# Kernel optimization log

Measured on AMD Instinct MI355X. Metric: run time of the kernel, lower is better.

## Reference

```python
import jax, jax.numpy as jnp
import numpy as np

EPS = 1e-6  # flax nnx LayerNorm default

def _ln(x):
    # LayerNorm without scale/bias
    m = jnp.mean(x, axis=-1, keepdims=True)
    v = jnp.mean(jnp.square(x - m), axis=-1, keepdims=True)
    return (x - m) * jax.lax.rsqrt(v + EPS)

def _modulate(x, shift, scale):
    return x * (1.0 + scale[:, None]) + shift[:, None]

def setup_inputs() -> dict:
    key = jax.random.key(0)
    B, S, H, NH = 8, 1024, 1024, 16
    ks = jax.random.split(key, 12)
    s = lambda k, sh: jax.random.normal(k, sh, dtype=jnp.float32) * 0.02
    return {
        "x": jax.random.normal(ks[0], (B, S, H), dtype=jnp.float32),
        "c": jax.random.normal(ks[1], (B, H), dtype=jnp.float32),
        "w_ada": s(ks[2], (H, 6 * H)),
        "b_ada": jnp.zeros((6 * H,), dtype=jnp.float32),
        "w_qkv": s(ks[3], (H, 3 * H)),
        "w_proj": s(ks[4], (H, H)),
        "b_proj": jnp.zeros((H,), dtype=jnp.float32),
        "w_mlp1": s(ks[5], (H, 4 * H)),
        "b_mlp1": jnp.zeros((4 * H,), dtype=jnp.float32),
        "w_mlp2": s(ks[6], (4 * H, H)),
        "b_mlp2": jnp.zeros((H,), dtype=jnp.float32),
    }

def reference(x, c, w_ada, b_ada, w_qkv, w_proj, b_proj, w_mlp1, b_mlp1, w_mlp2, b_mlp2):
    B, S, H = x.shape
    NH = 16
    CH = H // NH
    # adaLN modulation: silu -> Linear
    cmod = jax.nn.silu(c) @ w_ada + b_ada  # [B, 6H]
    shift_msa, scale_msa, gate_msa, shift_mlp, scale_mlp, gate_mlp = jnp.split(cmod, 6, axis=-1)
    # attention branch
    x_mod = _modulate(_ln(x), shift_msa, scale_msa)
    qkv = x_mod @ w_qkv  # [B, S, 3H]
    k, q, v = jnp.split(qkv, 3, axis=-1)  # note source order: k, q, v
    k = k.reshape(B, S, NH, CH)
    q = q.reshape(B, S, NH, CH)
    v = v.reshape(B, S, NH, CH)
    q = q / CH  # faithful: divide by head_dim (not sqrt)
    w = jnp.einsum('bqhc,bkhc->bhqk', q, k).astype(jnp.float32)
    w = jax.nn.softmax(w, axis=-1)
    y = jnp.einsum('bhqk,bkhc->bqhc', w, v).reshape(B, S, H)
    attn_x = y @ w_proj + b_proj
    x = x + gate_msa[:, None] * attn_x
    # MLP branch
    x_mod2 = _modulate(_ln(x), shift_mlp, scale_mlp)
    h = jax.nn.gelu(x_mod2 @ w_mlp1 + b_mlp1)
    mlp_x = h @ w_mlp2 + b_mlp2
    x = x + gate_mlp[:, None] * mlp_x
    return x
```

## Files before the change

kernel.cpp:

```cpp
#include <hip/hip_runtime.h>
#include <stdint.h>

typedef unsigned short u16;
using bf16x8 = __attribute__((ext_vector_type(8))) __bf16;
using f32x4  = __attribute__((ext_vector_type(4))) float;

#define MFMA16(a,b,c) __builtin_amdgcn_mfma_f32_16x16x32_bf16((a),(b),(c),0,0,0)

__device__ __forceinline__ u16 f2bf(float f) {
  union { float f; uint32_t u; } v; v.f = f;
  uint32_t r = v.u + 0x7FFFu + ((v.u >> 16) & 1u);
  return (u16)(r >> 16);
}
__device__ __forceinline__ float bf2f(u16 u) {
  union { uint32_t u; float f; } v; v.u = ((uint32_t)u) << 16;
  return v.f;
}

__device__ __forceinline__ void gload_lds16(const void* g, void* l) {
  typedef const __attribute__((address_space(1))) void* gp_t;
  typedef __attribute__((address_space(3))) void* lp_t;
  __builtin_amdgcn_global_load_lds((gp_t)(uintptr_t)g,
                                   (lp_t)(uint32_t)(uintptr_t)l, 16, 0, 0);
}

__global__ __launch_bounds__(256)
void prep_k(const float* __restrict__ w_qkv, const float* __restrict__ w_proj,
            const float* __restrict__ w_mlp1, const float* __restrict__ w_mlp2,
            u16* __restrict__ oq, u16* __restrict__ op,
            u16* __restrict__ o1, u16* __restrict__ o2,
            const float* __restrict__ c, const float* __restrict__ w_ada,
            float* __restrict__ partial) {
  int bid = blockIdx.x;
  if (bid >= 3072) {
    bid -= 3072;
    const int jb = bid % 24, ks = bid / 24;
    const int j = jb * 256 + threadIdx.x;
    __shared__ float sil[8][32];
    {
      int b = threadIdx.x >> 5, kk = threadIdx.x & 31;
      float v = c[b * 1024 + ks * 32 + kk];
      sil[b][kk] = v / (1.f + __expf(-v));
    }
    __syncthreads();
    float acc[8] = {0,0,0,0,0,0,0,0};
#pragma unroll 8
    for (int kk = 0; kk < 32; ++kk) {
      float wv = w_ada[(size_t)(ks * 32 + kk) * 6144 + j];
#pragma unroll
      for (int b = 0; b < 8; ++b) acc[b] += sil[b][kk] * wv;
    }
#pragma unroll
    for (int b = 0; b < 8; ++b)
      partial[((size_t)ks * 8 + b) * 6144 + j] = acc[b];
    return;
  }
  const float* in; u16* out; int K, N, lo = 0, hi = 0;
  float scale = 1.0f;
  if (bid < 768)       { in = w_qkv;  out = oq; K = 1024; N = 3072;
                         lo = 1024; hi = 2048; scale = 1.0f / 64.0f; }
  else if (bid < 1024) { in = w_proj; out = op; K = 1024; N = 1024; bid -= 768; }
  else if (bid < 2048) { in = w_mlp1; out = o1; K = 1024; N = 4096; bid -= 1024; }
  else                 { in = w_mlp2; out = o2; K = 4096; N = 1024; bid -= 2048; }
  const int nbx = N >> 6;
  const int n0 = (bid % nbx) * 64, k0 = (bid / nbx) * 64;
  __shared__ u16 t[64][65];
#pragma unroll
  for (int i = 0; i < 16; ++i) {
    int idx = i * 256 + threadIdx.x;
    int r = idx >> 6, cc = idx & 63;
    float v = in[(size_t)(k0 + r) * N + n0 + cc];
    int n = n0 + cc;
    if (n >= lo && n < hi) v *= scale;
    t[r][cc] = f2bf(v);
  }
  __syncthreads();
#pragma unroll
  for (int i = 0; i < 16; ++i) {
    int idx = i * 256 + threadIdx.x;
    int r = idx >> 6, cc = idx & 63;
    out[(size_t)(n0 + r) * K + k0 + cc] = t[cc][r];
  }
}

__global__ __launch_bounds__(256)
void adaln_red_k(const float* __restrict__ partial, const float* __restrict__ bias,
                 float* __restrict__ cmod) {
  int g = blockIdx.x * 256 + threadIdx.x;
  int j = g % 6144;
  float s = bias[j];
#pragma unroll 8
  for (int ks = 0; ks < 32; ++ks)
    s += partial[(size_t)ks * 8 * 6144 + g];
  cmod[g] = s;
}

__global__ __launch_bounds__(256)
void lnmod_k(const float* __restrict__ x, const float* __restrict__ cmod,
             int shift_off, int scale_off, u16* __restrict__ out) {
  int row = blockIdx.x;
  int b = row >> 10;
  const float4* xr = (const float4*)(x + (size_t)row * 1024);
  float4 v = xr[threadIdx.x];
  float s = v.x + v.y + v.z + v.w;
  float sq = v.x * v.x + v.y * v.y + v.z * v.z + v.w * v.w;
#pragma unroll
  for (int m = 32; m >= 1; m >>= 1) {
    s  += __shfl_xor(s, m);
    sq += __shfl_xor(sq, m);
  }
  __shared__ float ss[4], ssq[4];
  int wave = threadIdx.x >> 6, lane = threadIdx.x & 63;
  if (lane == 0) { ss[wave] = s; ssq[wave] = sq; }
  __syncthreads();
  s  = ss[0] + ss[1] + ss[2] + ss[3];
  sq = ssq[0] + ssq[1] + ssq[2] + ssq[3];
  float mean = s * (1.f / 1024.f);
  float var  = sq * (1.f / 1024.f) - mean * mean;
  float rstd = rsqrtf(var + 1e-6f);
  int col = threadIdx.x * 4;
  const float* sh = cmod + (size_t)b * 6144 + shift_off + col;
  const float* sc = cmod + (size_t)b * 6144 + scale_off + col;
  float xv[4] = {v.x, v.y, v.z, v.w};
  union { u16 o[4]; uint64_t u; } pk;
#pragma unroll
  for (int j = 0; j < 4; ++j)
    pk.o[j] = f2bf((xv[j] - mean) * rstd * (1.f + sc[j]) + sh[j]);
  *(uint64_t*)(out + (size_t)row * 1024 + col) = pk.u;
}

__global__ __launch_bounds__(256)
void lnmodb_k(const u16* __restrict__ x, const float* __restrict__ cmod,
              int shift_off, int scale_off, u16* __restrict__ out) {
  int row = blockIdx.x;
  int b = row >> 10;
  ushort4 v4 = *(const ushort4*)(x + (size_t)row * 1024 + threadIdx.x * 4);
  float xv[4] = {bf2f(v4.x), bf2f(v4.y), bf2f(v4.z), bf2f(v4.w)};
  float s = xv[0] + xv[1] + xv[2] + xv[3];
  float sq = xv[0]*xv[0] + xv[1]*xv[1] + xv[2]*xv[2] + xv[3]*xv[3];
#pragma unroll
  for (int m = 32; m >= 1; m >>= 1) {
    s  += __shfl_xor(s, m);
    sq += __shfl_xor(sq, m);
  }
  __shared__ float ss[4], ssq[4];
  int wave = threadIdx.x >> 6, lane = threadIdx.x & 63;
  if (lane == 0) { ss[wave] = s; ssq[wave] = sq; }
  __syncthreads();
  s  = ss[0] + ss[1] + ss[2] + ss[3];
  sq = ssq[0] + ssq[1] + ssq[2] + ssq[3];
  float mean = s * (1.f / 1024.f);
  float var  = sq * (1.f / 1024.f) - mean * mean;
  float rstd = rsqrtf(var + 1e-6f);
  int col = threadIdx.x * 4;
  const float* sh = cmod + (size_t)b * 6144 + shift_off + col;
  const float* sc = cmod + (size_t)b * 6144 + scale_off + col;
  union { u16 o[4]; uint64_t u; } pk;
#pragma unroll
  for (int j = 0; j < 4; ++j)
    pk.o[j] = f2bf((xv[j] - mean) * rstd * (1.f + sc[j]) + sh[j]);
  *(uint64_t*)(out + (size_t)row * 1024 + col) = pk.u;
}

__device__ __forceinline__ float gelu_f(float x) {
  float z = 1.5957691216057308f * (x + 0.044715f * x * x * x);
  return x / (1.f + __expf(-z));
}

template <int EP>
__global__ __launch_bounds__(256)
void gemm_k(const u16* __restrict__ A, const u16* __restrict__ Bt,
            int N, int K,
            const float* __restrict__ bias, const void* __restrict__ residp,
            const float* __restrict__ gate, void* __restrict__ outp) {
  __shared__ __align__(16) u16 lds[3][2][128 * 32];
  const int bn = blockIdx.x, bm = blockIdx.y;
  const int tid = threadIdx.x;
  const int wave = tid >> 6, lane = tid & 63;
  const int l15 = lane & 15, lhi = lane >> 4;
  const int wr = wave >> 1, wc = wave & 1;
  f32x4 acc[4][4] = {};
  const int nkt = K >> 5;
  const size_t arow0 = (size_t)bm * 128;
  const size_t brow0 = (size_t)bn * 128;

  auto stage = [&](int buf, int kt) {
#pragma unroll
    for (int i = 0; i < 2; ++i) {
      int c = (i * 4 + wave) * 64 + lane;
      int row = c >> 2;
      int kc = (c & 3) ^ ((row >> 1) & 3);
      gload_lds16(A  + (arow0 + row) * K + (size_t)kt * 32 + kc * 8,
                  &lds[buf][0][(i * 4 + wave) * 512]);
      gload_lds16(Bt + (brow0 + row) * K + (size_t)kt * 32 + kc * 8,
                  &lds[buf][1][(i * 4 + wave) * 512]);
    }
  };
  auto compute = [&](int buf) {
    bf16x8 af[4], bfr[4];
#pragma unroll
    for (int m = 0; m < 4; ++m) {
      int r = wr * 64 + m * 16 + l15;
      af[m] = *(const bf16x8*)&lds[buf][0][r * 32 + (lhi ^ ((r >> 1) & 3)) * 8];
    }
#pragma unroll
    for (int n = 0; n < 4; ++n) {
      int r = wc * 64 + n * 16 + l15;
      bfr[n] = *(const bf16x8*)&lds[buf][1][r * 32 + (lhi ^ ((r >> 1) & 3)) * 8];
    }
#pragma unroll
    for (int m = 0; m < 4; ++m)
#pragma unroll
      for (int n = 0; n < 4; ++n)
        acc[m][n] = MFMA16(af[m], bfr[n], acc[m][n]);
  };

  stage(0, 0);
  stage(1, 1);
  asm volatile("s_waitcnt vmcnt(4)" ::: "memory");
  __builtin_amdgcn_s_barrier();
  asm volatile("" ::: "memory");

  for (int t = 0; t < nkt; ++t) {
    const int cur = t % 3;
    const bool pf2 = (t + 2 < nkt);
    if (pf2) stage((t + 2) % 3, t + 2);
    compute(cur);
    if (t + 1 < nkt) {
      if (pf2) asm volatile("s_waitcnt vmcnt(4)" ::: "memory");
      else     asm volatile("s_waitcnt vmcnt(0)" ::: "memory");
      __builtin_amdgcn_s_barrier();
      asm volatile("" ::: "memory");
    }
  }

#pragma unroll
  for (int m = 0; m < 4; ++m) {
    int row = bm * 128 + wr * 64 + m * 16 + lhi * 4;
#pragma unroll
    for (int n = 0; n < 4; ++n) {
      int col = bn * 128 + wc * 64 + n * 16 + l15;
      if (EP == 0 && col >= 2048) {
        int h = (col - 2048) >> 6, ch = (col - 2048) & 63;
        int b = row >> 10, s0 = row & 1023;
        u16* vt = (u16*)residp;
        union { u16 o[4]; uint64_t u; } pk;
#pragma unroll
        for (int r = 0; r < 4; ++r) pk.o[r] = f2bf(acc[m][n][r]);
        *(uint64_t*)&vt[((size_t)(b * 16 + h) * 64 + ch) * 1024 + s0] = pk.u;
        continue;
      }
#pragma unroll
      for (int r = 0; r < 4; ++r) {
        int rr = row + r;
        float v = acc[m][n][r];
        if (EP == 0) {
          ((u16*)outp)[(size_t)rr * N + col] = f2bf(v);
        } else if (EP == 1) {
          ((u16*)outp)[(size_t)rr * N + col] = f2bf(gelu_f(v + bias[col]));
        } else if (EP == 2) {
          float t2 = v + bias[col];
          int b = rr >> 10;
          float res = ((const float*)residp)[(size_t)rr * N + col];
          ((u16*)outp)[(size_t)rr * N + col] =
              f2bf(res + gate[(size_t)b * 6144 + col] * t2);
        } else {
          float t2 = v + bias[col];
          int b = rr >> 10;
          float res = bf2f(((const u16*)residp)[(size_t)rr * N + col]);
          ((float*)outp)[(size_t)rr * N + col] = res + gate[(size_t)b * 6144 + col] * t2;
        }
      }
    }
  }
}

__global__ __launch_bounds__(256)
void attn_k(const u16* __restrict__ qkv, const u16* __restrict__ vt,
            u16* __restrict__ y) {
  int bid0 = blockIdx.x + 16 * (blockIdx.y + 16 * blockIdx.z);
  int swz = (bid0 & 7) * 256 + (bid0 >> 3);
  const int qt = swz & 15, h = (swz >> 4) & 15, b = swz >> 8;
  const int tid = threadIdx.x, wave = tid >> 6, lane = tid & 63;
  const int l15 = lane & 15, lhi = lane >> 4;
  __shared__ __align__(16) u16 Qs[64 * 64];
  __shared__ __align__(16) u16 Ks[2][64 * 64];
  __shared__ __align__(16) u16 Vs[2][64 * 64];
  __shared__ __align__(16) u16 Ps[64 * 64];
  const size_t qrow0 = (size_t)b * 1024 + qt * 64;
  const size_t krow0 = (size_t)b * 1024;
  const size_t vrow0 = (size_t)(b * 16 + h) * 64;

  auto stageQ = [&]() {
#pragma unroll
    for (int i = 0; i < 2; ++i) {
      int c = (i * 4 + wave) * 64 + lane;
      int r = c >> 3, j = (c & 7) ^ (r & 7);
      gload_lds16(qkv + (qrow0 + r) * 3072 + 1024 + h * 64 + j * 8,
                  &Qs[(i * 4 + wave) * 512]);
    }
  };
  auto stageKV = [&](int buf, int kt) {
#pragma unroll
    for (int i = 0; i < 2; ++i) {
      int c = (i * 4 + wave) * 64 + lane;
      int r = c >> 3, j = (c & 7) ^ (r & 7);
      gload_lds16(qkv + (krow0 + kt * 64 + r) * 3072 + h * 64 + j * 8,
                  &Ks[buf][(i * 4 + wave) * 512]);
      gload_lds16(vt + (vrow0 + r) * 1024 + kt * 64 + j * 8,
                  &Vs[buf][(i * 4 + wave) * 512]);
    }
  };
  auto ldb = [](const u16* base, int row, int cc) -> bf16x8 {
    return *(const bf16x8*)&base[row * 64 + ((cc ^ (row & 7)) << 3)];
  };

  stageQ();
  stageKV(0, 0);
  __syncthreads();
  bf16x8 qf[2];
  qf[0] = ldb(Qs, wave * 16 + l15, lhi);
  qf[1] = ldb(Qs, wave * 16 + l15, 4 + lhi);

  bf16x8 ones;
#pragma unroll
  for (int j = 0; j < 8; ++j) ones[j] = (__bf16)1.0f;

  f32x4 o[5] = {};

  for (int kt = 0; kt < 16; ++kt) {
    int cur = kt & 1;
    if (kt < 15) stageKV(cur ^ 1, kt + 1);
    f32x4 sf[4] = {};
    __builtin_amdgcn_s_setprio(1);
#pragma unroll
    for (int n = 0; n < 4; ++n) {
      bf16x8 k0 = ldb(Ks[cur], n * 16 + l15, lhi);
      bf16x8 k1 = ldb(Ks[cur], n * 16 + l15, 4 + lhi);
      sf[n] = MFMA16(qf[0], k0, sf[n]);
      sf[n] = MFMA16(qf[1], k1, sf[n]);
    }
    __builtin_amdgcn_s_setprio(0);
#pragma unroll
    for (int r = 0; r < 4; ++r) {
      int row = wave * 16 + lhi * 4 + r;
      int rb = row * 64, sw = (row & 7) << 3;
      Ps[rb + (l15 ^ sw)]        = f2bf(__expf(sf[0][r]));
      Ps[rb + ((l15 + 16) ^ sw)] = f2bf(__expf(sf[1][r]));
      Ps[rb + ((l15 + 32) ^ sw)] = f2bf(__expf(sf[2][r]));
      Ps[rb + ((l15 + 48) ^ sw)] = f2bf(__expf(sf[3][r]));
    }
    bf16x8 pf0 = ldb(Ps, wave * 16 + l15, lhi);
    bf16x8 pf1 = ldb(Ps, wave * 16 + l15, 4 + lhi);
    __builtin_amdgcn_s_setprio(1);
#pragma unroll
    for (int n = 0; n < 4; ++n) {
      bf16x8 v0 = ldb(Vs[cur], n * 16 + l15, lhi);
      bf16x8 v1 = ldb(Vs[cur], n * 16 + l15, 4 + lhi);
      o[n] = MFMA16(pf0, v0, o[n]);
      o[n] = MFMA16(pf1, v1, o[n]);
    }
    o[4] = MFMA16(pf0, ones, o[4]);
    o[4] = MFMA16(pf1, ones, o[4]);
    __builtin_amdgcn_s_setprio(0);
    __syncthreads();
  }
#pragma unroll
  for (int r = 0; r < 4; ++r) {
    float inv = 1.0f / o[4][r];
    size_t yrow = (qrow0 + wave * 16 + lhi * 4 + r) * 1024 + h * 64 + l15;
    y[yrow]      = f2bf(o[0][r] * inv);
    y[yrow + 16] = f2bf(o[1][r] * inv);
    y[yrow + 32] = f2bf(o[2][r] * inv);
    y[yrow + 48] = f2bf(o[3][r] * inv);
  }
}

extern "C" void kernel_launch(void* const* d_in, const int* in_sizes, int n_in,
                              void* d_out, int out_size, void* d_ws, size_t ws_size,
                              hipStream_t stream) {
  const float* x      = (const float*)d_in[0];
  const float* c      = (const float*)d_in[1];
  const float* w_ada  = (const float*)d_in[2];
  const float* b_ada  = (const float*)d_in[3];
  const float* w_qkv  = (const float*)d_in[4];
  const float* w_proj = (const float*)d_in[5];
  const float* b_proj = (const float*)d_in[6];
  const float* w_mlp1 = (const float*)d_in[7];
  const float* b_mlp1 = (const float*)d_in[8];
  const float* w_mlp2 = (const float*)d_in[9];
  const float* b_mlp2 = (const float*)d_in[10];
  float* out = (float*)d_out;

  char* ws = (char*)d_ws;
  size_t off = 0;
  auto alloc = [&](size_t bytes) {
    void* p = ws + off;
    off += (bytes + 255) & ~(size_t)255;
    return p;
  };
  float* cmod  = (float*)alloc((size_t)8 * 6144 * 4);
  float* apart = (float*)alloc((size_t)32 * 8 * 6144 * 4);
  u16* wqkvT   = (u16*)alloc((size_t)3072 * 1024 * 2);
  u16* wprojT  = (u16*)alloc((size_t)1024 * 1024 * 2);
  u16* wmlp1T  = (u16*)alloc((size_t)4096 * 1024 * 2);
  u16* wmlp2T  = (u16*)alloc((size_t)1024 * 4096 * 2);
  u16* xmod    = (u16*)alloc((size_t)8192 * 1024 * 2);
  u16* qkv     = (u16*)alloc((size_t)8192 * 3072 * 2);
  u16* vt      = (u16*)alloc((size_t)8 * 16 * 64 * 1024 * 2);
  u16* x1      = (u16*)alloc((size_t)8192 * 1024 * 2);
  u16* hbuf    = (u16*)alloc((size_t)8192 * 4096 * 2);
  u16* ybuf  = xmod;
  u16* xmod2 = qkv;

  prep_k<<<3840, 256, 0, stream>>>(w_qkv, w_proj, w_mlp1, w_mlp2,
                                   wqkvT, wprojT, wmlp1T, wmlp2T,
                                   c, w_ada, apart);
  adaln_red_k<<<192, 256, 0, stream>>>(apart, b_ada, cmod);
  lnmod_k<<<8192, 256, 0, stream>>>(x, cmod, 0, 1024, xmod);
  gemm_k<0><<<dim3(3072 / 128, 8192 / 128), 256, 0, stream>>>(
      xmod, wqkvT, 3072, 1024, nullptr, vt, nullptr, qkv);
  attn_k<<<dim3(16, 16, 8), 256, 0, stream>>>(qkv, vt, ybuf);
  gemm_k<2><<<dim3(1024 / 128, 8192 / 128), 256, 0, stream>>>(
      ybuf, wprojT, 1024, 1024, b_proj, x, cmod + 2048, x1);
  lnmodb_k<<<8192, 256, 0, stream>>>(x1, cmod, 3072, 4096, xmod2);
  gemm_k<1><<<dim3(4096 / 128, 8192 / 128), 256, 0, stream>>>(
      xmod2, wmlp1T, 4096, 1024, b_mlp1, nullptr, nullptr, hbuf);
  gemm_k<3><<<dim3(1024 / 128, 8192 / 128), 256, 0, stream>>>(
      hbuf, wmlp2T, 1024, 4096, b_mlp2, x1, cmod + 5120, out);
}
```

Measured before the change: 388.4 us.

## Load GEMM A fragments directly from global into registers, keep only B in LDS

The GEMM kernel stops staging the A tile in shared memory. Each wave now loads its A fragments straight from global memory into registers, while B is still staged through LDS. The three-buffer pipeline with explicit vmcnt waits becomes a double buffer using __syncthreads, unrolled by two. This cuts LDS footprint and LDS read traffic, but A is re-read from global or L2 by both column waves, the global loads are less coalesced, and latency hiding is shallower.

```diff
diff --git a/kernel.cpp b/kernel.cpp
--- a/kernel.cpp
+++ b/kernel.cpp
@@ -173,7 +173,7 @@
             int N, int K,
             const float* __restrict__ bias, const void* __restrict__ residp,
             const float* __restrict__ gate, void* __restrict__ outp) {
-  __shared__ __align__(16) u16 lds[3][2][128 * 32];
+  __shared__ __align__(16) u16 Bs[2][128 * 32];
   const int bn = blockIdx.x, bm = blockIdx.y;
   const int tid = threadIdx.x;
   const int wave = tid >> 6, lane = tid & 63;
@@ -184,30 +184,31 @@
   const size_t arow0 = (size_t)bm * 128;
   const size_t brow0 = (size_t)bn * 128;
 
-  auto stage = [&](int buf, int kt) {
+  const u16* abase[4];
+#pragma unroll
+  for (int m = 0; m < 4; ++m)
+    abase[m] = A + (arow0 + wr * 64 + m * 16 + l15) * (size_t)K + lhi * 8;
+
+  auto stageB = [&](int buf, int kt) {
 #pragma unroll
     for (int i = 0; i < 2; ++i) {
-      int c = (i * 4 + wave) * 64 + lane;
-      int row = c >> 2;
-      int kc = (c & 3) ^ ((row >> 1) & 3);
-      gload_lds16(A  + (arow0 + row) * K + (size_t)kt * 32 + kc * 8,
-                  &lds[buf][0][(i * 4 + wave) * 512]);
+      int cch = (i * 4 + wave) * 64 + lane;
+      int row = cch >> 2;
+      int kc = (cch & 3) ^ ((row >> 1) & 3);
       gload_lds16(Bt + (brow0 + row) * K + (size_t)kt * 32 + kc * 8,
-                  &lds[buf][1][(i * 4 + wave) * 512]);
-    }
-  };
-  auto compute = [&](int buf) {
-    bf16x8 af[4], bfr[4];
-#pragma unroll
-    for (int m = 0; m < 4; ++m) {
-      int r = wr * 64 + m * 16 + l15;
-      af[m] = *(const bf16x8*)&lds[buf][0][r * 32 + (lhi ^ ((r >> 1) & 3)) * 8];
-    }
-#pragma unroll
-    for (int n = 0; n < 4; ++n) {
-      int r = wc * 64 + n * 16 + l15;
-      bfr[n] = *(const bf16x8*)&lds[buf][1][r * 32 + (lhi ^ ((r >> 1) & 3)) * 8];
-    }
+                  &Bs[buf][(i * 4 + wave) * 512]);
+    }
+  };
+  int offB[4];
+#pragma unroll
+  for (int n = 0; n < 4; ++n) {
+    int r = wc * 64 + n * 16 + l15;
+    offB[n] = r * 32 + (lhi ^ ((r >> 1) & 3)) * 8;
+  }
+  auto computeB = [&](int buf, const bf16x8* af) {
+    bf16x8 bfr[4];
+#pragma unroll
+    for (int n = 0; n < 4; ++n) bfr[n] = *(const bf16x8*)&Bs[buf][offB[n]];
 #pragma unroll
     for (int m = 0; m < 4; ++m)
 #pragma unroll
@@ -215,23 +216,27 @@
         acc[m][n] = MFMA16(af[m], bfr[n], acc[m][n]);
   };
 
-  stage(0, 0);
-  stage(1, 1);
-  asm volatile("s_waitcnt vmcnt(4)" ::: "memory");
-  __builtin_amdgcn_s_barrier();
-  asm volatile("" ::: "memory");
-
-  for (int t = 0; t < nkt; ++t) {
-    const int cur = t % 3;
-    const bool pf2 = (t + 2 < nkt);
-    if (pf2) stage((t + 2) % 3, t + 2);
-    compute(cur);
-    if (t + 1 < nkt) {
-      if (pf2) asm volatile("s_waitcnt vmcnt(4)" ::: "memory");
-      else     asm volatile("s_waitcnt vmcnt(0)" ::: "memory");
-      __builtin_amdgcn_s_barrier();
-      asm volatile("" ::: "memory");
-    }
+  bf16x8 afA[4], afB[4];
+#pragma unroll
+  for (int m = 0; m < 4; ++m) afA[m] = *(const bf16x8*)(abase[m]);
+  stageB(0, 0);
+  __syncthreads();
+
+  for (int t = 0; t < nkt; t += 2) {
+    stageB(1, t + 1);
+#pragma unroll
+    for (int m = 0; m < 4; ++m)
+      afB[m] = *(const bf16x8*)(abase[m] + (t + 1) * 32);
+    computeB(0, afA);
+    __syncthreads();
+    if (t + 2 < nkt) {
+      stageB(0, t + 2);
+#pragma unroll
+      for (int m = 0; m < 4; ++m)
+        afA[m] = *(const bf16x8*)(abase[m] + (t + 2) * 32);
+    }
+    computeB(1, afB);
+    __syncthreads();
   }
 
 #pragma unroll
```

Result: slower. 619.3 us (+59.4%).

## Add 256x256-tile 8-wave ping-pong GEMM for MLP1 with GELU epilogue

Applied to the files above, without the earlier changes.

Adds a new GEMM kernel with 256x256 output tiles, 512 threads (8 waves), and a double-buffered global-to-LDS pipeline that interleaves LDS fragment loads, prefetch of k+2 tiles, and MFMA phases under barriers and s_setprio. It replaces the 128x128 gemm_k<1> for the MLP1 projection (8192x4096x1024), which is the largest GEMM. The larger tile is meant to raise arithmetic intensity and cut global and LDS traffic per FLOP. In exchange it runs one workgroup per CU with 512 blocks total, and the epilogue writes scalar bf16 stores.

```diff
diff --git a/kernel.cpp b/kernel.cpp
--- a/kernel.cpp
+++ b/kernel.cpp
@@ -275,6 +275,165 @@
   }
 }
 
+__global__ __launch_bounds__(512, 1)
+void gemm8_k(const u16* __restrict__ A, const u16* __restrict__ Bt,
+             int N, int K,
+             const float* __restrict__ bias, u16* __restrict__ outp) {
+  __shared__ __align__(16) u16 As[2][256 * 64];
+  __shared__ __align__(16) u16 Bs[2][256 * 64];
+  const int nwg = gridDim.x * gridDim.y;
+  int bid = blockIdx.y * gridDim.x + blockIdx.x;
+  int swz = (bid & 7) * (nwg >> 3) + (bid >> 3);
+  const int bn = swz % gridDim.x, bm = swz / gridDim.x;
+  const int tid = threadIdx.x;
+  const int wave = tid >> 6, lane = tid & 63;
+  const int l15 = lane & 15, lhi = lane >> 4;
+  const int wm = wave >> 2, wn = wave & 3;
+  const int nkt = K >> 6;
+  const size_t arow0 = (size_t)bm * 256;
+  const size_t brow0 = (size_t)bn * 256;
+
+  f32x4 acc[2][4][4] = {};
+
+  auto stage_half = [&](const u16* mat, size_t row0, u16* dst, int kt) {
+    const u16* src = mat + row0 * K + (size_t)kt * 64;
+#pragma unroll
+    for (int i = 0; i < 2; ++i) {
+      int q = i * 512 + tid;
+      int r = q >> 3, cc = (q & 7) ^ (r & 7);
+      gload_lds16(src + (size_t)r * K + cc * 8, dst + (i * 8 + wave) * 512);
+    }
+  };
+  auto lda = [&](int cur, int row, int kh) -> bf16x8 {
+    int cc = (kh * 4 + lhi) ^ (row & 7);
+    return *(const bf16x8*)&As[cur][row * 64 + cc * 8];
+  };
+  auto ldbf = [&](int cur, int row, int kh) -> bf16x8 {
+    int cc = (kh * 4 + lhi) ^ (row & 7);
+    return *(const bf16x8*)&Bs[cur][row * 64 + cc * 8];
+  };
+
+#define PH_BAR()  do { asm volatile("" ::: "memory"); __builtin_amdgcn_s_barrier(); \
+                       asm volatile("" ::: "memory"); } while (0)
+#define PH_LGKM() do { asm volatile("s_waitcnt lgkmcnt(0)" ::: "memory"); \
+                       __builtin_amdgcn_sched_barrier(0); } while (0)
+
+  stage_half(A,  arow0,       &As[0][0],        0);
+  stage_half(A,  arow0 + 128, &As[0][128 * 64], 0);
+  stage_half(Bt, brow0,       &Bs[0][0],        0);
+  stage_half(Bt, brow0 + 128, &Bs[0][128 * 64], 0);
+  stage_half(A,  arow0,       &As[1][0],        1);
+  stage_half(A,  arow0 + 128, &As[1][128 * 64], 1);
+  stage_half(Bt, brow0,       &Bs[1][0],        1);
+  stage_half(Bt, brow0 + 128, &Bs[1][128 * 64], 1);
+  asm volatile("s_waitcnt vmcnt(8)" ::: "memory");
+  PH_BAR();
+
+  bf16x8 afr[4][2], bfr01[2][2], bfr23[2][2];
+  for (int kt = 0; kt < nkt; ++kt) {
+    const int cur = kt & 1;
+    const bool pf2 = (kt + 2 < nkt);
+
+#pragma unroll
+    for (int m = 0; m < 4; ++m) {
+      int r = wm * 128 + m * 16 + l15;
+      afr[m][0] = lda(cur, r, 0); afr[m][1] = lda(cur, r, 1);
+    }
+#pragma unroll
+    for (int n = 0; n < 2; ++n) {
+      int r = wn * 64 + n * 16 + l15;
+      bfr01[n][0] = ldbf(cur, r, 0); bfr01[n][1] = ldbf(cur, r, 1);
+    }
+    PH_BAR(); PH_LGKM();
+    __builtin_amdgcn_s_setprio(1);
+#pragma unroll
+    for (int m = 0; m < 4; ++m)
+#pragma unroll
+      for (int n = 0; n < 2; ++n) {
+        acc[0][m][n] = MFMA16(afr[m][0], bfr01[n][0], acc[0][m][n]);
+        acc[0][m][n] = MFMA16(afr[m][1], bfr01[n][1], acc[0][m][n]);
+      }
+    __builtin_amdgcn_s_setprio(0);
+    PH_BAR();
+
+#pragma unroll
+    for (int n = 0; n < 2; ++n) {
+      int r = wn * 64 + (n + 2) * 16 + l15;
+      bfr23[n][0] = ldbf(cur, r, 0); bfr23[n][1] = ldbf(cur, r, 1);
+    }
+    PH_BAR(); PH_LGKM();
+    __builtin_amdgcn_s_setprio(1);
+#pragma unroll
+    for (int m = 0; m < 4; ++m)
+#pragma unroll
+      for (int n = 0; n < 2; ++n) {
+        acc[0][m][n + 2] = MFMA16(afr[m][0], bfr23[n][0], acc[0][m][n + 2]);
+        acc[0][m][n + 2] = MFMA16(afr[m][1], bfr23[n][1], acc[0][m][n + 2]);
+      }
+    __builtin_amdgcn_s_setprio(0);
+    PH_BAR();
+
+#pragma unroll
+    for (int m = 0; m < 4; ++m) {
+      int r = wm * 128 + 64 + m * 16 + l15;
+      afr[m][0] = lda(cur, r, 0); afr[m][1] = lda(cur, r, 1);
+    }
+    if (pf2) {
+      stage_half(Bt, brow0,       &Bs[cur][0],        kt + 2);
+      stage_half(Bt, brow0 + 128, &Bs[cur][128 * 64], kt + 2);
+    }
+    PH_BAR(); PH_LGKM();
+    __builtin_amdgcn_s_setprio(1);
+#pragma unroll
+    for (int m = 0; m < 4; ++m)
+#pragma unroll
+      for (int n = 0; n < 2; ++n) {
+        acc[1][m][n] = MFMA16(afr[m][0], bfr01[n][0], acc[1][m][n]);
+        acc[1][m][n] = MFMA16(afr[m][1], bfr01[n][1], acc[1][m][n]);
+      }
+    __builtin_amdgcn_s_setprio(0);
+    PH_BAR();
+
+    if (pf2) {
+      stage_half(A, arow0,       &As[cur][0],        kt + 2);
+      stage_half(A, arow0 + 128, &As[cur][128 * 64], kt + 2);
+    }
+    PH_BAR();
+    __builtin_amdgcn_s_setprio(1);
+#pragma unroll
+    for (int m = 0; m < 4; ++m)
+#pragma unroll
+      for (int n = 0; n < 2; ++n) {
+        acc[1][m][n + 2] = MFMA16(afr[m][0], bfr23[n][0], acc[1][m][n + 2]);
+        acc[1][m][n + 2] = MFMA16(afr[m][1], bfr23[n][1], acc[1][m][n + 2]);
+      }
+    __builtin_amdgcn_s_setprio(0);
+    if (kt + 1 < nkt) {
+      if (pf2) asm volatile("s_waitcnt vmcnt(8)" ::: "memory");
+      else     asm volatile("s_waitcnt vmcnt(0)" ::: "memory");
+      PH_BAR();
+    }
+  }
+#undef PH_BAR
+#undef PH_LGKM
+
+#pragma unroll
+  for (int mh = 0; mh < 2; ++mh)
+#pragma unroll
+    for (int m = 0; m < 4; ++m) {
+      int row = bm * 256 + wm * 128 + mh * 64 + m * 16 + lhi * 4;
+#pragma unroll
+      for (int n = 0; n < 4; ++n) {
+        int col = bn * 256 + wn * 64 + n * 16 + l15;
+#pragma unroll
+        for (int r = 0; r < 4; ++r) {
+          int rr = row + r;
+          outp[(size_t)rr * N + col] = f2bf(gelu_f(acc[mh][m][n][r] + bias[col]));
+        }
+      }
+    }
+}
+
 __global__ __launch_bounds__(256)
 void attn_k(const u16* __restrict__ qkv, const u16* __restrict__ vt,
             u16* __restrict__ y) {
@@ -424,8 +583,8 @@
   gemm_k<2><<<dim3(1024 / 128, 8192 / 128), 256, 0, stream>>>(
       ybuf, wprojT, 1024, 1024, b_proj, x, cmod + 2048, x1);
   lnmodb_k<<<8192, 256, 0, stream>>>(x1, cmod, 3072, 4096, xmod2);
-  gemm_k<1><<<dim3(4096 / 128, 8192 / 128), 256, 0, stream>>>(
-      xmod2, wmlp1T, 4096, 1024, b_mlp1, nullptr, nullptr, hbuf);
+  gemm8_k<<<dim3(4096 / 256, 8192 / 256), 512, 0, stream>>>(
+      xmod2, wmlp1T, 4096, 1024, b_mlp1, hbuf);
   gemm_k<3><<<dim3(1024 / 128, 8192 / 128), 256, 0, stream>>>(
       hbuf, wmlp2T, 1024, 4096, b_mlp2, x1, cmod + 5120, out);
 }
```

Result: faster. 374.4 us (median of 2 runs) (-3.6%).
